# Performance work log

Measured on AMD Instinct MI355X. Metric: run time of the kernel, lower is better.

## Reference

```python
import jax, jax.numpy as jnp
import numpy as np

S = 2048        # seqlen_sum (packed tokens)
DIM = 4096
N_HEADS = 32
N_KV_HEADS = 8
HEAD_DIM = 128
ROPE_THETA = 10000.0


def setup_inputs() -> dict:
    key = jax.random.key(0)
    ks = jax.random.split(key, 5)
    x = jax.random.normal(ks[0], (S, DIM), dtype=jnp.float32)
    # true RoPE frequencies: freqs_cis = exp(i * pos * theta^{-2j/d})
    inv_freq = ROPE_THETA ** (-jnp.arange(0, HEAD_DIM, 2, dtype=jnp.float32) / HEAD_DIM)  # [64]
    angles = jnp.arange(S, dtype=jnp.float32)[:, None] * inv_freq[None, :]               # [S,64]
    freqs_cos = jnp.cos(angles)
    freqs_sin = jnp.sin(angles)
    scale = 0.02
    wq = jax.random.normal(ks[1], (DIM, N_HEADS * HEAD_DIM), dtype=jnp.float32) * scale
    wk = jax.random.normal(ks[2], (DIM, N_KV_HEADS * HEAD_DIM), dtype=jnp.float32) * scale
    wv = jax.random.normal(ks[3], (DIM, N_KV_HEADS * HEAD_DIM), dtype=jnp.float32) * scale
    wo = jax.random.normal(ks[4], (N_HEADS * HEAD_DIM, DIM), dtype=jnp.float32) * scale
    return {"x": x, "freqs_cos": freqs_cos, "freqs_sin": freqs_sin,
            "wq": wq, "wk": wk, "wv": wv, "wo": wo}


def _apply_rope(t, cos, sin):
    # t: [S, H, D]; pairs (t0,t1) along last dim form complex numbers (torch view_as_complex)
    tr = t.reshape(t.shape[0], t.shape[1], -1, 2)
    t0, t1 = tr[..., 0], tr[..., 1]
    c = cos[:, None, :]  # [S,1,D/2]
    s = sin[:, None, :]
    o0 = t0 * c - t1 * s
    o1 = t0 * s + t1 * c
    return jnp.stack([o0, o1], axis=-1).reshape(t.shape)


def reference(x, freqs_cos, freqs_sin, wq, wk, wv, wo):
    repeats = N_HEADS // N_KV_HEADS
    xq = (x @ wq).reshape(S, N_HEADS, HEAD_DIM)
    xk = (x @ wk).reshape(S, N_KV_HEADS, HEAD_DIM)
    xv = (x @ wv).reshape(S, N_KV_HEADS, HEAD_DIM)
    xq = _apply_rope(xq, freqs_cos, freqs_sin)
    xk = _apply_rope(xk, freqs_cos, freqs_sin)
    # GQA: repeat_interleave KV heads (cache=None path -> key/val = xk/xv)
    key = jnp.repeat(xk, repeats, axis=1)  # [S, N_HEADS, D]
    val = jnp.repeat(xv, repeats, axis=1)
    scale = HEAD_DIM ** -0.5
    scores = jnp.einsum('qhd,khd->hqk', xq, key) * scale   # [H,S,S]
    attn = jax.nn.softmax(scores, axis=-1)
    out = jnp.einsum('hqk,khd->qhd', attn, val)            # [S,H,D]
    return out.reshape(S, N_HEADS * HEAD_DIM) @ wo
```

## Files before the change

### kernel.cpp

```cpp
#include <hip/hip_runtime.h>

#define S_LEN 2048
#define DIM   4096
#define NH    32
#define NKV   8
#define HD    128
#define QKV_LD 6144
#define KOFF 4096
#define VOFF 5120

typedef __attribute__((ext_vector_type(8))) __bf16 bf16x8;
typedef __attribute__((ext_vector_type(4))) float  floatx4;

union U8 { unsigned short u[8]; bf16x8 v; int4 i4; };
union U32x4 { unsigned int u[4]; bf16x8 v; };

__device__ inline unsigned short f2bf(float f) {
  unsigned int u = __float_as_uint(f);
  u += 0x7fff + ((u >> 16) & 1);
  return (unsigned short)(u >> 16);
}
__device__ inline float bf2f(unsigned short h) {
  return __uint_as_float(((unsigned int)h) << 16);
}

__device__ inline floatx4 mfma16(bf16x8 a, bf16x8 b, floatx4 c) {
  return __builtin_amdgcn_mfma_f32_16x16x32_bf16(a, b, c, 0, 0, 0);
}

typedef __attribute__((address_space(1))) void GV;
typedef __attribute__((address_space(3))) void LV;
__device__ inline void gload_lds16(const unsigned short* g, unsigned short* l) {
  __builtin_amdgcn_global_load_lds((GV*)g, (LV*)l, 16, 0, 0);
}

template<int N> __device__ __forceinline__ void vmcnt_wait() {
  if constexpr (N == 8)      asm volatile("s_waitcnt vmcnt(8)" ::: "memory");
  else if constexpr (N == 6) asm volatile("s_waitcnt vmcnt(6)" ::: "memory");
  else if constexpr (N == 4) asm volatile("s_waitcnt vmcnt(4)" ::: "memory");
  else if constexpr (N == 2) asm volatile("s_waitcnt vmcnt(2)" ::: "memory");
  else                       asm volatile("s_waitcnt vmcnt(0)" ::: "memory");
}

__global__ __launch_bounds__(256) void transpose_cvt(
    const float* __restrict__ in, unsigned short* __restrict__ outT, int K, int N)
{
  __shared__ float t[32][33];
  const int n0 = blockIdx.x * 32, k0 = blockIdx.y * 32;
  const int tx = threadIdx.x & 31, ty = threadIdx.x >> 5;
#pragma unroll
  for (int i = 0; i < 32; i += 8)
    t[ty + i][tx] = in[(size_t)(k0 + ty + i) * N + n0 + tx];
  __syncthreads();
#pragma unroll
  for (int i = 0; i < 32; i += 8)
    outT[(size_t)(n0 + ty + i) * K + k0 + tx] = f2bf(t[tx][ty + i]);
}

__global__ __launch_bounds__(256) void cvt_f32_bf16(
    const float* __restrict__ in, unsigned short* __restrict__ out)
{
  int i = (blockIdx.x * 256 + threadIdx.x) * 8;
  float4 a = *(const float4*)(in + i);
  float4 b = *(const float4*)(in + i + 4);
  U8 t;
  t.u[0] = f2bf(a.x); t.u[1] = f2bf(a.y); t.u[2] = f2bf(a.z); t.u[3] = f2bf(a.w);
  t.u[4] = f2bf(b.x); t.u[5] = f2bf(b.y); t.u[6] = f2bf(b.z); t.u[7] = f2bf(b.w);
  *(int4*)(out + i) = t.i4;
}

template<bool C_F32>
__global__ __launch_bounds__(256) void gemm_bt(
    const unsigned short* __restrict__ A,
    const unsigned short* __restrict__ Bt,
    void* __restrict__ C_, int M, int N, int K)
{
  __shared__ __align__(16) unsigned short As[128 * 32];
  __shared__ __align__(16) unsigned short Bs[128 * 32];

  const int tid  = threadIdx.x;
  const int wave = tid >> 6;
  const int lane = tid & 63;
  const int quad = lane >> 4;
  const int l16  = lane & 15;
  const int m0 = blockIdx.y * 128, n0 = blockIdx.x * 128;
  const int mw = (wave & 1) * 64, nw = (wave >> 1) * 64;

  floatx4 acc[4][4] = {};

  for (int k0 = 0; k0 < K; k0 += 32) {
#pragma unroll
    for (int p = 0; p < 2; p++) {
      int c = wave * 128 + p * 64 + lane;
      gload_lds16(A  + (size_t)(m0 + (c >> 2)) * K + k0 + (c & 3) * 8,
                  As + (wave * 128 + p * 64) * 8);
      gload_lds16(Bt + (size_t)(n0 + (c >> 2)) * K + k0 + (c & 3) * 8,
                  Bs + (wave * 128 + p * 64) * 8);
    }
    __syncthreads();

    bf16x8 af[4], bf[4];
#pragma unroll
    for (int mt = 0; mt < 4; mt++)
      af[mt] = *(const bf16x8*)(As + (mw + mt * 16 + l16) * 32 + quad * 8);
#pragma unroll
    for (int nt = 0; nt < 4; nt++)
      bf[nt] = *(const bf16x8*)(Bs + (nw + nt * 16 + l16) * 32 + quad * 8);
#pragma unroll
    for (int mt = 0; mt < 4; mt++)
#pragma unroll
      for (int nt = 0; nt < 4; nt++)
        acc[mt][nt] = mfma16(af[mt], bf[nt], acc[mt][nt]);
    __syncthreads();
  }

#pragma unroll
  for (int mt = 0; mt < 4; mt++)
#pragma unroll
    for (int nt = 0; nt < 4; nt++)
#pragma unroll
      for (int i = 0; i < 4; i++) {
        int r = m0 + mw + mt * 16 + quad * 4 + i;
        int c = n0 + nw + nt * 16 + l16;
        if (C_F32) ((float*)C_)[(size_t)r * N + c] = acc[mt][nt][i];
        else ((unsigned short*)C_)[(size_t)r * N + c] = f2bf(acc[mt][nt][i]);
      }
}

template<bool C_F32>
__global__ __launch_bounds__(512, 2) void gemm8(
    const unsigned short* __restrict__ A,
    const unsigned short* __restrict__ Bt,
    void* __restrict__ C_, int M, int N, int K)
{
  __shared__ __align__(16) unsigned short As[2][256 * 64];
  __shared__ __align__(16) unsigned short Bs[2][256 * 64];

  const int nwg  = gridDim.x * gridDim.y;
  const int bid0 = blockIdx.y * gridDim.x + blockIdx.x;
  const int wg   = (bid0 & 7) * (nwg >> 3) + (bid0 >> 3);
  const int bx = wg % gridDim.x, by = wg / gridDim.x;
  const int m0 = by * 256, n0 = bx * 256;

  const int tid  = threadIdx.x;
  const int wave = tid >> 6, lane = tid & 63;
  const int quad = lane >> 4, l16 = lane & 15;
  const int wm = wave >> 2, wn = wave & 3;

  floatx4 acc[8][4] = {};
  bf16x8 af[4][2];
  bf16x8 bfr[2][2][2];

#define STAGE_A8(buf_, mq_, kt_) do {                                           \
    _Pragma("unroll")                                                           \
    for (int s = 0; s < 2; s++) {                                               \
      int row = s * 128 + (mq_) * 64 + (tid >> 3);                              \
      gload_lds16(A + (size_t)(m0 + row) * K + (kt_) * 64                       \
                    + (((tid & 7) ^ (row & 7)) * 8),                            \
                  &As[buf_][(s * 128 + (mq_) * 64 + wave * 8) * 64]);           \
    } } while (0)

#define STAGE_B8(buf_, nq_, kt_) do {                                           \
    _Pragma("unroll")                                                           \
    for (int s = 0; s < 2; s++) {                                               \
      int c = s * 512 + tid;                                                    \
      int row = (c >> 8) * 64 + (nq_) * 32 + ((c >> 3) & 31);                   \
      gload_lds16(Bt + (size_t)(n0 + row) * K + (kt_) * 64                      \
                    + (((tid & 7) ^ (row & 7)) * 8),                            \
                  &Bs[buf_][((s * 2 + (wave >> 2)) * 64 + (nq_) * 32            \
                            + (wave & 3) * 8) * 64]);                           \
    } } while (0)

#define LOAD_AF8(buf_, mq_) do {                                                \
    _Pragma("unroll")                                                           \
    for (int m = 0; m < 4; m++)                                                 \
    _Pragma("unroll")                                                           \
      for (int ks = 0; ks < 2; ks++) {                                          \
        int row = wm * 128 + (mq_) * 64 + m * 16 + l16;                         \
        af[m][ks] = *(const bf16x8*)(&As[buf_][row * 64                         \
                       + (((ks * 4 + quad) ^ (l16 & 7)) * 8)]);                 \
      } } while (0)

#define LOAD_BF8(buf_, nq_) do {                                                \
    _Pragma("unroll")                                                           \
    for (int n = 0; n < 2; n++)                                                 \
    _Pragma("unroll")                                                           \
      for (int ks = 0; ks < 2; ks++) {                                          \
        int row = wn * 64 + (nq_) * 32 + n * 16 + l16;                          \
        bfr[nq_][n][ks] = *(const bf16x8*)(&Bs[buf_][row * 64                   \
                       + (((ks * 4 + quad) ^ (l16 & 7)) * 8)]);                 \
      } } while (0)

#define MFMA_Q8(mq_, nq_) do {                                                  \
    __builtin_amdgcn_s_setprio(1);                                              \
    _Pragma("unroll")                                                           \
    for (int ks = 0; ks < 2; ks++)                                              \
    _Pragma("unroll")                                                           \
      for (int m = 0; m < 4; m++)                                               \
      _Pragma("unroll")                                                         \
        for (int n = 0; n < 2; n++)                                             \
          acc[(mq_) * 4 + m][(nq_) * 2 + n] = mfma16(af[m][ks],                 \
              bfr[nq_][n][ks], acc[(mq_) * 4 + m][(nq_) * 2 + n]);              \
    __builtin_amdgcn_s_setprio(0);                                              \
  } while (0)

#define BAR_MID() do { __builtin_amdgcn_s_barrier();                            \
    asm volatile("s_waitcnt lgkmcnt(0)" ::: "memory");                          \
    __builtin_amdgcn_sched_barrier(0); } while (0)

#define GATE(n_) do { vmcnt_wait<n_>();                                         \
    __builtin_amdgcn_sched_barrier(0);                                          \
    __builtin_amdgcn_s_barrier(); } while (0)

#define ENDP() __builtin_amdgcn_s_barrier()

  const int NIT = K >> 7;

  STAGE_A8(0, 0, 0); STAGE_B8(0, 0, 0); STAGE_B8(0, 1, 0); STAGE_A8(0, 1, 0);
  vmcnt_wait<4>();
  __builtin_amdgcn_s_barrier();

  for (int i = 0; i < NIT; i++) {
    const int t1 = 2 * i + 1, t2 = 2 * i + 2;
    const bool more = (i + 1 < NIT);
    LOAD_AF8(0, 0); LOAD_BF8(0, 0);
    STAGE_A8(1, 0, t1);
    BAR_MID(); MFMA_Q8(0, 0); GATE(4);
    LOAD_BF8(0, 1);
    STAGE_B8(1, 0, t1);
    BAR_MID(); MFMA_Q8(0, 1); GATE(4);
    LOAD_AF8(0, 1);
    STAGE_B8(1, 1, t1);
    BAR_MID(); MFMA_Q8(1, 1); ENDP();
    STAGE_A8(1, 1, t1);
    BAR_MID(); MFMA_Q8(1, 0); GATE(4);
    LOAD_AF8(1, 0); LOAD_BF8(1, 0);
    if (more) STAGE_A8(0, 0, t2);
    BAR_MID(); MFMA_Q8(0, 0);
    if (more) GATE(4); else GATE(2);
    LOAD_BF8(1, 1);
    if (more) STAGE_B8(0, 0, t2);
    BAR_MID(); MFMA_Q8(0, 1);
    if (more) GATE(4); else GATE(0);
    LOAD_AF8(1, 1);
    if (more) STAGE_B8(0, 1, t2);
    BAR_MID(); MFMA_Q8(1, 1); ENDP();
    if (more) STAGE_A8(0, 1, t2);
    BAR_MID(); MFMA_Q8(1, 0);
    if (more) GATE(4); else ENDP();
  }

#undef STAGE_A8
#undef STAGE_B8
#undef LOAD_AF8
#undef LOAD_BF8
#undef MFMA_Q8
#undef BAR_MID
#undef GATE
#undef ENDP

#pragma unroll
  for (int mq = 0; mq < 2; mq++)
#pragma unroll
    for (int m = 0; m < 4; m++)
#pragma unroll
      for (int nq = 0; nq < 2; nq++)
#pragma unroll
        for (int n = 0; n < 2; n++)
#pragma unroll
          for (int i2 = 0; i2 < 4; i2++) {
            int r = m0 + wm * 128 + mq * 64 + m * 16 + quad * 4 + i2;
            int c = n0 + wn * 64 + nq * 32 + n * 16 + l16;
            float v = acc[mq * 4 + m][nq * 2 + n][i2];
            if (C_F32) ((float*)C_)[(size_t)r * N + c] = v;
            else ((unsigned short*)C_)[(size_t)r * N + c] = f2bf(v);
          }
}

__global__ __launch_bounds__(256) void rope_kernel(
    unsigned short* __restrict__ qkv,
    const float* __restrict__ fcos, const float* __restrict__ fsin)
{
  int idx = blockIdx.x * 256 + threadIdx.x;
  int p = idx & 63;
  int t = idx >> 6;
  int h = t % (NH + NKV);
  int s = t / (NH + NKV);

  float c  = fcos[s * 64 + p];
  float sn = fsin[s * 64 + p];
  const float qs = 0.08838834764831845f;

  unsigned short* base;
  float m;
  if (h < NH) { base = qkv + (size_t)s * QKV_LD + h * HD + p * 2; m = qs; }
  else { base = qkv + (size_t)s * QKV_LD + KOFF + (h - NH) * HD + p * 2; m = 1.f; }

  unsigned int both = *(const unsigned int*)base;
  float t0 = bf2f((unsigned short)(both & 0xffff));
  float t1 = bf2f((unsigned short)(both >> 16));
  unsigned int o0 = f2bf((t0 * c - t1 * sn) * m);
  unsigned int o1 = f2bf((t0 * sn + t1 * c) * m);
  *(unsigned int*)base = o0 | (o1 << 16);
}

__global__ __launch_bounds__(256) void vtrans_kernel(
    const unsigned short* __restrict__ qkv, unsigned short* __restrict__ vt)
{
  __shared__ unsigned short t[32][34];
  const int s0 = blockIdx.x * 32;
  const int d0 = blockIdx.y * 32;
  const int tx = threadIdx.x & 31, ty = threadIdx.x >> 5;
#pragma unroll
  for (int i = 0; i < 32; i += 8)
    t[ty + i][tx] = qkv[(size_t)(s0 + ty + i) * QKV_LD + VOFF + d0 + tx];
  __syncthreads();
#pragma unroll
  for (int i = 0; i < 32; i += 8)
    vt[(size_t)(d0 + ty + i) * S_LEN + s0 + tx] = t[tx][ty + i];
}

__global__ __launch_bounds__(256, 2) void attn_kernel(
    const unsigned short* __restrict__ qkv,
    const unsigned short* __restrict__ vt,
    unsigned short* __restrict__ o)
{
  __shared__ __align__(16) unsigned short Ks[2][64 * 136];
  __shared__ __align__(16) unsigned short Vs[2][128 * 72];

  const int h    = blockIdx.x;
  const int qblk = blockIdx.y;
  const int kvh  = h >> 2;
  const int tid  = threadIdx.x;
  const int lane = tid & 63;
  const int quad = lane >> 4;
  const int l16  = lane & 15;
  const int wave = tid >> 6;
  const int qr   = qblk * 128 + wave * 16;

  bf16x8 qf[2][4];
#pragma unroll
  for (int mt = 0; mt < 2; mt++)
#pragma unroll
    for (int ks = 0; ks < 4; ks++)
      qf[mt][ks] = *(const bf16x8*)(qkv + (size_t)(qr + mt * 64 + l16) * QKV_LD
                                    + h * HD + ks * 32 + quad * 8);

  floatx4 accO[2][8] = {};
  float l_i[2] = {0.f, 0.f};

  int4 pk[4], pv4[4];
#define LOAD_TILE(kb_) do {                                                     \
    _Pragma("unroll")                                                           \
    for (int j = 0; j < 4; j++) {                                               \
      int c = tid + 256 * j;                                                    \
      pk[j] = *(const int4*)(qkv + (size_t)((kb_) * 64 + (c >> 4)) * QKV_LD     \
                              + KOFF + kvh * HD + (c & 15) * 8);                \
      pv4[j] = *(const int4*)(vt + (size_t)(kvh * HD + (c >> 3)) * S_LEN        \
                              + (kb_) * 64 + (c & 7) * 8);                      \
    } } while (0)
#define STORE_TILE(b_) do {                                                     \
    _Pragma("unroll")                                                           \
    for (int j = 0; j < 4; j++) {                                               \
      int c = tid + 256 * j;                                                    \
      *(int4*)(Ks[b_] + (c >> 4) * 136 + (c & 15) * 8) = pk[j];                 \
      *(int4*)(Vs[b_] + (c >> 3) * 72 + (c & 7) * 8) = pv4[j];                  \
    } } while (0)

  LOAD_TILE(0);
  STORE_TILE(0);
  __syncthreads();

  const int srcA = ((quad & 1) << 5) | l16;
  const bool hi  = (quad & 2);

  for (int kb = 0; kb < S_LEN / 64; kb++) {
    const int cur = kb & 1;
    if (kb + 1 < S_LEN / 64) LOAD_TILE(kb + 1);

    const unsigned short* Ksc = Ks[cur];
    const unsigned short* Vsc = Vs[cur];

    floatx4 sacc[2][4] = {};
    __builtin_amdgcn_s_setprio(1);
#pragma unroll
    for (int ks = 0; ks < 4; ks++)
#pragma unroll
      for (int nt = 0; nt < 4; nt++) {
        bf16x8 kf = *(const bf16x8*)(Ksc + (nt * 16 + l16) * 136 + ks * 32 + quad * 8);
        sacc[0][nt] = mfma16(kf, qf[0][ks], sacc[0][nt]);
        sacc[1][nt] = mfma16(kf, qf[1][ks], sacc[1][nt]);
      }
    __builtin_amdgcn_s_setprio(0);

    unsigned int wp[2][2][4];
#pragma unroll
    for (int mt = 0; mt < 2; mt++) {
      float ls = 0.f;
#pragma unroll
      for (int nt = 0; nt < 4; nt++) {
        float e0 = __expf(sacc[mt][nt][0]);
        float e1 = __expf(sacc[mt][nt][1]);
        float e2 = __expf(sacc[mt][nt][2]);
        float e3 = __expf(sacc[mt][nt][3]);
        ls += (e0 + e1) + (e2 + e3);
        wp[mt][0][nt] = (unsigned int)f2bf(e0) | ((unsigned int)f2bf(e1) << 16);
        wp[mt][1][nt] = (unsigned int)f2bf(e2) | ((unsigned int)f2bf(e3) << 16);
      }
      l_i[mt] += ls;
    }

#pragma unroll
    for (int k2 = 0; k2 < 2; k2++) {
      bf16x8 paf[2];
#pragma unroll
      for (int mt = 0; mt < 2; mt++) {
        const int ntl = k2 * 2, nth = k2 * 2 + 1;
        unsigned int a0 = __shfl((int)wp[mt][0][ntl], srcA, 64);
        unsigned int b0 = __shfl((int)wp[mt][0][nth], srcA, 64);
        unsigned int a1 = __shfl((int)wp[mt][1][ntl], srcA, 64);
        unsigned int b1 = __shfl((int)wp[mt][1][nth], srcA, 64);
        unsigned int a2 = __shfl((int)wp[mt][0][ntl], srcA + 16, 64);
        unsigned int b2 = __shfl((int)wp[mt][0][nth], srcA + 16, 64);
        unsigned int a3 = __shfl((int)wp[mt][1][ntl], srcA + 16, 64);
        unsigned int b3 = __shfl((int)wp[mt][1][nth], srcA + 16, 64);
        U32x4 pw;
        pw.u[0] = hi ? b0 : a0;
        pw.u[1] = hi ? b1 : a1;
        pw.u[2] = hi ? b2 : a2;
        pw.u[3] = hi ? b3 : a3;
        paf[mt] = pw.v;
      }
      __builtin_amdgcn_s_setprio(1);
#pragma unroll
      for (int dt = 0; dt < 8; dt++) {
        bf16x8 vf = *(const bf16x8*)(Vsc + (dt * 16 + l16) * 72 + k2 * 32 + quad * 8);
        accO[0][dt] = mfma16(paf[0], vf, accO[0][dt]);
        accO[1][dt] = mfma16(paf[1], vf, accO[1][dt]);
      }
      __builtin_amdgcn_s_setprio(0);
    }

    if (kb + 1 < S_LEN / 64) STORE_TILE(cur ^ 1);
    __syncthreads();
  }

#pragma unroll
  for (int mt = 0; mt < 2; mt++) {
    l_i[mt] += __shfl_xor(l_i[mt], 16, 64);
    l_i[mt] += __shfl_xor(l_i[mt], 32, 64);
  }

#pragma unroll
  for (int mt = 0; mt < 2; mt++) {
    float lq[4];
#pragma unroll
    for (int i = 0; i < 4; i++) lq[i] = __shfl(l_i[mt], quad * 4 + i, 64);
#pragma unroll
    for (int dt = 0; dt < 8; dt++)
#pragma unroll
      for (int i = 0; i < 4; i++) {
        float val = accO[mt][dt][i] / lq[i];
        o[(size_t)(qr + mt * 64 + quad * 4 + i) * (NH * HD) + h * HD + dt * 16 + l16]
            = f2bf(val);
      }
  }
#undef LOAD_TILE
#undef STORE_TILE
}

extern "C" void kernel_launch(void* const* d_in, const int* in_sizes, int n_in,
                              void* d_out, int out_size, void* d_ws, size_t ws_size,
                              hipStream_t stream)
{
  const float* x    = (const float*)d_in[0];
  const float* fcos = (const float*)d_in[1];
  const float* fsin = (const float*)d_in[2];
  const float* wq   = (const float*)d_in[3];
  const float* wk   = (const float*)d_in[4];
  const float* wv   = (const float*)d_in[5];
  const float* wo   = (const float*)d_in[6];
  float* out = (float*)d_out;

  unsigned short* ws = (unsigned short*)d_ws;
  unsigned short* xb   = ws;
  unsigned short* wT   = xb   + (size_t)S_LEN * DIM;
  unsigned short* woT  = wT   + (size_t)QKV_LD * DIM;
  unsigned short* qkv  = woT  + (size_t)DIM * (NH * HD);
  unsigned short* vt   = qkv  + (size_t)S_LEN * QKV_LD;
  unsigned short* attn = vt   + (size_t)S_LEN * (NKV * HD);

  cvt_f32_bf16<<<(S_LEN * DIM) / (256 * 8), 256, 0, stream>>>(x, xb);
  transpose_cvt<<<dim3(DIM / 32, DIM / 32),        256, 0, stream>>>(wq, wT, DIM, DIM);
  transpose_cvt<<<dim3((NKV * HD) / 32, DIM / 32), 256, 0, stream>>>(wk, wT + (size_t)KOFF * DIM, DIM, NKV * HD);
  transpose_cvt<<<dim3((NKV * HD) / 32, DIM / 32), 256, 0, stream>>>(wv, wT + (size_t)VOFF * DIM, DIM, NKV * HD);
  transpose_cvt<<<dim3(DIM / 32, (NH * HD) / 32),  256, 0, stream>>>(wo, woT, NH * HD, DIM);

  gemm8<false>
      <<<dim3(QKV_LD / 256, S_LEN / 256), 512, 0, stream>>>(xb, wT, qkv, S_LEN, QKV_LD, DIM);

  rope_kernel<<<(S_LEN * (NH + NKV) * 64) / 256, 256, 0, stream>>>(qkv, fcos, fsin);
  vtrans_kernel<<<dim3(S_LEN / 32, (NKV * HD) / 32), 256, 0, stream>>>(qkv, vt);

  attn_kernel<<<dim3(NH, S_LEN / 128), 256, 0, stream>>>(qkv, vt, attn);

  gemm_bt<true><<<dim3(DIM / 128, S_LEN / 128), 256, 0, stream>>>(attn, woT, out, S_LEN, DIM, NH * HD);
}
```

Baseline: 567.3 us.

## Deepen gemm8 prefetch to a full tile ahead and remap workgroups per XCD

The gemm8 prologue now stages two K-tiles before the loop, and the loop restages each buffer only after that buffer has been consumed. Loads are issued one full tile ahead, and the vmcnt gates are adjusted to allow more outstanding global-to-LDS loads. This aims to hide more global memory latency behind MFMA work. The workgroup-to-tile mapping is also changed to a hardcoded XCD-aware layout (2x4 groups of 4x6 tiles), meant to improve L2 locality per XCD. That mapping assumes a specific grid shape (8 by 24 tiles) and would be wrong for other GEMM sizes.

```diff
diff --git a/kernel.cpp b/kernel.cpp
--- a/kernel.cpp
+++ b/kernel.cpp
@@ -35,11 +35,12 @@
 }
 
 template<int N> __device__ __forceinline__ void vmcnt_wait() {
-  if constexpr (N == 8)      asm volatile("s_waitcnt vmcnt(8)" ::: "memory");
-  else if constexpr (N == 6) asm volatile("s_waitcnt vmcnt(6)" ::: "memory");
-  else if constexpr (N == 4) asm volatile("s_waitcnt vmcnt(4)" ::: "memory");
-  else if constexpr (N == 2) asm volatile("s_waitcnt vmcnt(2)" ::: "memory");
-  else                       asm volatile("s_waitcnt vmcnt(0)" ::: "memory");
+  if constexpr (N == 12)      asm volatile("s_waitcnt vmcnt(12)" ::: "memory");
+  else if constexpr (N == 10) asm volatile("s_waitcnt vmcnt(10)" ::: "memory");
+  else if constexpr (N == 8)  asm volatile("s_waitcnt vmcnt(8)" ::: "memory");
+  else if constexpr (N == 4)  asm volatile("s_waitcnt vmcnt(4)" ::: "memory");
+  else if constexpr (N == 2)  asm volatile("s_waitcnt vmcnt(2)" ::: "memory");
+  else                        asm volatile("s_waitcnt vmcnt(0)" ::: "memory");
 }
 
 __global__ __launch_bounds__(256) void transpose_cvt(
@@ -136,10 +137,10 @@
   __shared__ __align__(16) unsigned short As[2][256 * 64];
   __shared__ __align__(16) unsigned short Bs[2][256 * 64];
 
-  const int nwg  = gridDim.x * gridDim.y;
   const int bid0 = blockIdx.y * gridDim.x + blockIdx.x;
-  const int wg   = (bid0 & 7) * (nwg >> 3) + (bid0 >> 3);
-  const int bx = wg % gridDim.x, by = wg / gridDim.x;
+  const int xcd = bid0 & 7, j = bid0 >> 3;
+  const int by = (xcd >> 2) * 4 + j / 6;
+  const int bx = (xcd & 3) * 6 + j % 6;
   const int m0 = by * 256, n0 = bx * 256;
 
   const int tid  = threadIdx.x;
@@ -217,37 +218,38 @@
   const int NIT = K >> 7;
 
   STAGE_A8(0, 0, 0); STAGE_B8(0, 0, 0); STAGE_B8(0, 1, 0); STAGE_A8(0, 1, 0);
-  vmcnt_wait<4>();
+  STAGE_A8(1, 0, 1); STAGE_B8(1, 0, 1); STAGE_B8(1, 1, 1); STAGE_A8(1, 1, 1);
+  vmcnt_wait<12>();
   __builtin_amdgcn_s_barrier();
 
   for (int i = 0; i < NIT; i++) {
-    const int t1 = 2 * i + 1, t2 = 2 * i + 2;
+    const int tE = 2 * i + 2, tO = 2 * i + 3;
     const bool more = (i + 1 < NIT);
     LOAD_AF8(0, 0); LOAD_BF8(0, 0);
-    STAGE_A8(1, 0, t1);
-    BAR_MID(); MFMA_Q8(0, 0); GATE(4);
+    BAR_MID(); MFMA_Q8(0, 0); GATE(10);
     LOAD_BF8(0, 1);
-    STAGE_B8(1, 0, t1);
-    BAR_MID(); MFMA_Q8(0, 1); GATE(4);
+    if (more) { STAGE_A8(0, 0, tE); STAGE_B8(0, 0, tE); }
+    BAR_MID(); MFMA_Q8(0, 1);
+    if (more) GATE(12); else GATE(8);
     LOAD_AF8(0, 1);
-    STAGE_B8(1, 1, t1);
+    if (more) STAGE_B8(0, 1, tE);
     BAR_MID(); MFMA_Q8(1, 1); ENDP();
-    STAGE_A8(1, 1, t1);
-    BAR_MID(); MFMA_Q8(1, 0); GATE(4);
+    if (more) STAGE_A8(0, 1, tE);
+    BAR_MID(); MFMA_Q8(1, 0);
+    if (more) GATE(12); else GATE(4);
     LOAD_AF8(1, 0); LOAD_BF8(1, 0);
-    if (more) STAGE_A8(0, 0, t2);
     BAR_MID(); MFMA_Q8(0, 0);
-    if (more) GATE(4); else GATE(2);
+    if (more) GATE(10); else GATE(2);
     LOAD_BF8(1, 1);
-    if (more) STAGE_B8(0, 0, t2);
+    if (more) { STAGE_A8(1, 0, tO); STAGE_B8(1, 0, tO); }
     BAR_MID(); MFMA_Q8(0, 1);
-    if (more) GATE(4); else GATE(0);
+    if (more) GATE(12); else GATE(0);
     LOAD_AF8(1, 1);
-    if (more) STAGE_B8(0, 1, t2);
+    if (more) STAGE_B8(1, 1, tO);
     BAR_MID(); MFMA_Q8(1, 1); ENDP();
-    if (more) STAGE_A8(0, 1, t2);
+    if (more) STAGE_A8(1, 1, tO);
     BAR_MID(); MFMA_Q8(1, 0);
-    if (more) GATE(4); else ENDP();
+    if (more) GATE(12); else ENDP();
   }
 
 #undef STAGE_A8
```

Measured after the change: 554.4 us. -2.3%, faster.
